# Kernel tuning notes

Hardware: AMD Instinct MI355X
Metric: run time of the kernel (lower is better)

The kernel has to match this reference:

```python
import jax, jax.numpy as jnp
import numpy as np
from jax import lax

B, T, I, H = 262144, 10, 1, 32


def setup_inputs() -> dict:
    key = jax.random.key(0)
    ks = jax.random.split(key, 7)
    s_ih = 1.0 / np.sqrt(H)
    return {
        "x": jax.random.normal(ks[0], (B, T, I), dtype=jnp.float32),
        "h0": jnp.zeros((1, B, H), dtype=jnp.float32),
        "Wih": jax.random.uniform(ks[1], (H, I), minval=-s_ih, maxval=s_ih, dtype=jnp.float32),
        "Whh": jax.random.uniform(ks[2], (H, H), minval=-s_ih, maxval=s_ih, dtype=jnp.float32),
        "bih": jax.random.uniform(ks[3], (H,), minval=-s_ih, maxval=s_ih, dtype=jnp.float32),
        "bhh": jax.random.uniform(ks[4], (H,), minval=-s_ih, maxval=s_ih, dtype=jnp.float32),
        "Wout": jax.random.uniform(ks[5], (1, H), minval=-s_ih, maxval=s_ih, dtype=jnp.float32),
        "bout": jax.random.uniform(ks[6], (1,), minval=-s_ih, maxval=s_ih, dtype=jnp.float32),
    }


def reference(x, h0, Wih, Whh, bih, bhh, Wout, bout):
    # Elman RNN: h_t = tanh(x_t Wih^T + bih + h_{t-1} Whh^T + bhh)
    # Precompute the input projection for all timesteps (batched GEMM),
    # then scan the sequential recurrence over T.
    xW = jnp.einsum("bti,hi->tbh", x, Wih) + (bih + bhh)  # [T,B,H]

    def step(h, xw_t):
        h_new = jnp.tanh(xw_t + h @ Whh.T)
        return h_new, h_new

    h_last, hs = lax.scan(step, h0[0], xW)  # hs: [T,B,H]
    r_out = jnp.swapaxes(hs, 0, 1)  # [B,T,H]
    outs = r_out @ Wout.T + bout    # fused linear head, [B,T,1]
    return outs, h_last[None]       # match (outs.view(-1,T,1), h_state[1,B,H])
```

## Files before the change

### kernel.cpp

```cpp
#include <hip/hip_runtime.h>


#define RNN_T 10
#define RNN_H 32

typedef __attribute__((ext_vector_type(4))) unsigned int u32x4;
typedef __attribute__((ext_vector_type(8))) short s16x8;
typedef __attribute__((ext_vector_type(16))) float f32x16;

static __device__ __forceinline__ float fast_tanh(float a) {
    float ez = __builtin_amdgcn_exp2f(a * 2.885390081777927f);
    float r  = __builtin_amdgcn_rcpf(ez + 1.0f);
    return fmaf(-2.0f, r, 1.0f);
}

static __device__ __forceinline__ unsigned pack_hi_pair(float f0, float f1) {
    return (__float_as_uint(f1) & 0xffff0000u) | (__float_as_uint(f0) >> 16);
}
static __device__ __forceinline__ float trunc_bf16_f32(float f) {
    return __uint_as_float(__float_as_uint(f) & 0xffff0000u);
}

static __device__ __forceinline__ f32x16 mfma_bf16(u32x4 a, u32x4 b, f32x16 c) {
    return __builtin_amdgcn_mfma_f32_32x32x16_bf16(
        __builtin_bit_cast(s16x8, a), __builtin_bit_cast(s16x8, b), c, 0, 0, 0);
}

static __device__ __forceinline__ void load_split8(const float* __restrict__ p,
                                                   u32x4& hi4, u32x4& lo4) {
    float4 w0 = *reinterpret_cast<const float4*>(p);
    float4 w1 = *reinterpret_cast<const float4*>(p + 4);
    float w[8] = {w0.x, w0.y, w0.z, w0.w, w1.x, w1.y, w1.z, w1.w};
    #pragma unroll
    for (int i = 0; i < 4; ++i) {
        float f0 = w[2 * i], f1 = w[2 * i + 1];
        hi4[i] = pack_hi_pair(f0, f1);
        lo4[i] = pack_hi_pair(f0 - trunc_bf16_f32(f0), f1 - trunc_bf16_f32(f1));
    }
}

__global__ __launch_bounds__(256) void rnn_mfma(
    const float* __restrict__ x,
    const float* __restrict__ h0,
    const float* __restrict__ Wih,
    const float* __restrict__ Whh,
    const float* __restrict__ bih,
    const float* __restrict__ bhh,
    const float* __restrict__ Wout,
    const float* __restrict__ bout,
    float* __restrict__ out,
    int B)
{
    const int tid  = threadIdx.x;
    const int lane = tid & 63;
    const int l31  = lane & 31;
    const int hi   = lane >> 5;
    const bool lo_lane = (hi == 0);
    const int wave = tid >> 6;
    const int tile = blockIdx.x * 4 + wave;
    const int b    = tile * 32 + l31;
    const int kb   = hi * 8;

    u32x4 A1h, A1l, A2h, A2l;
    load_split8(Whh + l31 * RNN_H + 0  + kb, A1h, A1l);
    load_split8(Whh + l31 * RNN_H + 16 + kb, A2h, A2l);

    u32x4 B1h, B1l, B2h, B2l;
    load_split8(h0 + (size_t)b * RNN_H + 0  + kb, B1h, B1l);
    load_split8(h0 + (size_t)b * RNN_H + 16 + kb, B2h, B2l);

    float wih_r[16], bias_r[16], wout_r[16];
    #pragma unroll
    for (int r = 0; r < 16; ++r) {
        int row = (r & 3) + 8 * (r >> 2) + 4 * hi;
        wih_r[r]  = Wih[row];
        bias_r[r] = bih[row] + bhh[row];
        wout_r[r] = Wout[row];
    }

    float xw[RNN_T];
    #pragma unroll
    for (int t = 0; t < RNN_T; ++t) xw[t] = x[(size_t)b * RNN_T + t];

    const float bo = bout[0];
    float h[16];

    #pragma unroll
    for (int t = 0; t < RNN_T; ++t) {
        f32x16 acc;
        #pragma unroll
        for (int r = 0; r < 16; ++r) acc[r] = fmaf(xw[t], wih_r[r], bias_r[r]);

        acc = mfma_bf16(A1h, B1h, acc);
        acc = mfma_bf16(A2h, B2h, acc);
        acc = mfma_bf16(A1h, B1l, acc);
        acc = mfma_bf16(A2h, B2l, acc);
        acc = mfma_bf16(A1l, B1h, acc);
        acc = mfma_bf16(A2l, B2h, acc);
        acc = mfma_bf16(A1l, B1l, acc);
        acc = mfma_bf16(A2l, B2l, acc);

        #pragma unroll
        for (int r = 0; r < 16; ++r) h[r] = fast_tanh(acc[r]);

        float o = 0.f;
        #pragma unroll
        for (int r = 0; r < 16; ++r) o = fmaf(h[r], wout_r[r], o);
        o += __shfl_xor(o, 32);
        if (lane < 32) out[(size_t)b * RNN_T + t] = o + bo;

        if (t < RNN_T - 1) {
            unsigned Sh[8], Sl[8];
            #pragma unroll
            for (int p = 0; p < 8; ++p) {
                float f0 = h[2 * p], f1 = h[2 * p + 1];
                Sh[p] = pack_hi_pair(f0, f1);
                Sl[p] = pack_hi_pair(f0 - trunc_bf16_f32(f0),
                                     f1 - trunc_bf16_f32(f1));
            }
            unsigned r0h = __shfl_xor(lo_lane ? Sh[2] : Sh[0], 32);
            unsigned r1h = __shfl_xor(lo_lane ? Sh[3] : Sh[1], 32);
            unsigned r2h = __shfl_xor(lo_lane ? Sh[6] : Sh[4], 32);
            unsigned r3h = __shfl_xor(lo_lane ? Sh[7] : Sh[5], 32);
            unsigned r0l = __shfl_xor(lo_lane ? Sl[2] : Sl[0], 32);
            unsigned r1l = __shfl_xor(lo_lane ? Sl[3] : Sl[1], 32);
            unsigned r2l = __shfl_xor(lo_lane ? Sl[6] : Sl[4], 32);
            unsigned r3l = __shfl_xor(lo_lane ? Sl[7] : Sl[5], 32);
            B1h[0] = lo_lane ? Sh[0] : r0h;  B1h[1] = lo_lane ? Sh[1] : r1h;
            B1h[2] = lo_lane ? r0h : Sh[2];  B1h[3] = lo_lane ? r1h : Sh[3];
            B2h[0] = lo_lane ? Sh[4] : r2h;  B2h[1] = lo_lane ? Sh[5] : r3h;
            B2h[2] = lo_lane ? r2h : Sh[6];  B2h[3] = lo_lane ? r3h : Sh[7];
            B1l[0] = lo_lane ? Sl[0] : r0l;  B1l[1] = lo_lane ? Sl[1] : r1l;
            B1l[2] = lo_lane ? r0l : Sl[2];  B1l[3] = lo_lane ? r1l : Sl[3];
            B2l[0] = lo_lane ? Sl[4] : r2l;  B2l[1] = lo_lane ? Sl[5] : r3l;
            B2l[2] = lo_lane ? r2l : Sl[6];  B2l[3] = lo_lane ? r3l : Sl[7];
        }
    }

    float* hl = out + (size_t)B * RNN_T + (size_t)b * RNN_H;
    #pragma unroll
    for (int q = 0; q < 4; ++q) {
        float4 v;
        v.x = h[4 * q + 0]; v.y = h[4 * q + 1];
        v.z = h[4 * q + 2]; v.w = h[4 * q + 3];
        *reinterpret_cast<float4*>(hl + 8 * q + 4 * hi) = v;
    }
}

extern "C" void kernel_launch(void* const* d_in, const int* in_sizes, int n_in,
                              void* d_out, int out_size, void* d_ws, size_t ws_size,
                              hipStream_t stream) {
    const float* x    = (const float*)d_in[0];
    const float* h0   = (const float*)d_in[1];
    const float* Wih  = (const float*)d_in[2];
    const float* Whh  = (const float*)d_in[3];
    const float* bih  = (const float*)d_in[4];
    const float* bhh  = (const float*)d_in[5];
    const float* Wout = (const float*)d_in[6];
    const float* bout = (const float*)d_in[7];
    float* out = (float*)d_out;

    const int B = in_sizes[1] / RNN_H;
    dim3 grid(B / 128);
    dim3 block(256);
    hipLaunchKernelGGL(rnn_mfma, grid, block, 0, stream,
                       x, h0, Wih, Whh, bih, bhh, Wout, bout, out, B);
}
```

Baseline: 134.4 us.

## Interleave two batch tiles per wave, use permlane32 swaps, drop lo*lo MFMA terms

Each wave now processes two 32-row batch tiles with interleaved MFMA chains, so the two independent dependency chains can hide MFMA and tanh latency. Cross-half exchanges move from shfl_xor with selects to v_permlane32_swap, and the two lowest-order bf16 split products (A_lo*B_lo) are dropped, leaving six MFMAs per tile instead of eight. The time loop is no longer unrolled, and x is prefetched one step ahead instead of loaded up front. The grid is halved. Dropping the lo*lo terms slightly reduces precision, and there are fewer waves to hide latency.

```diff
diff --git a/kernel.cpp b/kernel.cpp
--- a/kernel.cpp
+++ b/kernel.cpp
@@ -39,9 +39,22 @@
     }
 }
 
-__global__ __launch_bounds__(256) void rnn_mfma(
+static __device__ __forceinline__ void swap32(unsigned& xv, unsigned& yv) {
+    asm volatile("v_permlane32_swap_b32 %0, %1" : "+v"(xv), "+v"(yv));
+}
+
+static __device__ __forceinline__ void rebuild(const unsigned S[8],
+                                               u32x4& Bk1, u32x4& Bk2) {
+    unsigned a, b;
+    a = S[0]; b = S[2]; swap32(a, b); Bk1[0] = a; Bk1[2] = b;
+    a = S[1]; b = S[3]; swap32(a, b); Bk1[1] = a; Bk1[3] = b;
+    a = S[4]; b = S[6]; swap32(a, b); Bk2[0] = a; Bk2[2] = b;
+    a = S[5]; b = S[7]; swap32(a, b); Bk2[1] = a; Bk2[3] = b;
+}
+
+__global__ __launch_bounds__(256) void rnn_mfma2(
     const float* __restrict__ x,
-    const float* __restrict__ h0,
+    const float* __restrict__ hin,
     const float* __restrict__ Wih,
     const float* __restrict__ Whh,
     const float* __restrict__ bih,
@@ -55,19 +68,20 @@
     const int lane = tid & 63;
     const int l31  = lane & 31;
     const int hi   = lane >> 5;
-    const bool lo_lane = (hi == 0);
     const int wave = tid >> 6;
-    const int tile = blockIdx.x * 4 + wave;
-    const int b    = tile * 32 + l31;
+    const int b0   = (blockIdx.x * 8 + wave * 2) * 32 + l31;
+    const int b1   = b0 + 32;
     const int kb   = hi * 8;
 
     u32x4 A1h, A1l, A2h, A2l;
-    load_split8(Whh + l31 * RNN_H + 0  + kb, A1h, A1l);
+    load_split8(Whh + l31 * RNN_H + kb,      A1h, A1l);
     load_split8(Whh + l31 * RNN_H + 16 + kb, A2h, A2l);
 
-    u32x4 B1h, B1l, B2h, B2l;
-    load_split8(h0 + (size_t)b * RNN_H + 0  + kb, B1h, B1l);
-    load_split8(h0 + (size_t)b * RNN_H + 16 + kb, B2h, B2l);
+    u32x4 B1h0, B1l0, B2h0, B2l0, B1h1, B1l1, B2h1, B2l1;
+    load_split8(hin + (size_t)b0 * RNN_H + kb,      B1h0, B1l0);
+    load_split8(hin + (size_t)b0 * RNN_H + 16 + kb, B2h0, B2l0);
+    load_split8(hin + (size_t)b1 * RNN_H + kb,      B1h1, B1l1);
+    load_split8(hin + (size_t)b1 * RNN_H + 16 + kb, B2h1, B2l1);
 
     float wih_r[16], bias_r[16], wout_r[16];
     #pragma unroll
@@ -78,72 +92,83 @@
         wout_r[r] = Wout[row];
     }
 
-    float xw[RNN_T];
-    #pragma unroll
-    for (int t = 0; t < RNN_T; ++t) xw[t] = x[(size_t)b * RNN_T + t];
+    const float bo = bout[0];
+    const float* xp0 = x + (size_t)b0 * RNN_T;
+    const float* xp1 = x + (size_t)b1 * RNN_T;
+    float* op0 = out + (size_t)b0 * RNN_T;
+    float* op1 = out + (size_t)b1 * RNN_T;
 
-    const float bo = bout[0];
-    float h[16];
+    float h0r[16], h1r[16];
+    float xc0 = xp0[0], xc1 = xp1[0];
 
-    #pragma unroll
+    #pragma unroll 1
     for (int t = 0; t < RNN_T; ++t) {
-        f32x16 acc;
+        const int tn = (t < RNN_T - 1) ? t + 1 : t;
+        const float xn0 = xp0[tn], xn1 = xp1[tn];
+
+        f32x16 acc0, acc1;
         #pragma unroll
-        for (int r = 0; r < 16; ++r) acc[r] = fmaf(xw[t], wih_r[r], bias_r[r]);
-
-        acc = mfma_bf16(A1h, B1h, acc);
-        acc = mfma_bf16(A2h, B2h, acc);
-        acc = mfma_bf16(A1h, B1l, acc);
-        acc = mfma_bf16(A2h, B2l, acc);
-        acc = mfma_bf16(A1l, B1h, acc);
-        acc = mfma_bf16(A2l, B2h, acc);
-        acc = mfma_bf16(A1l, B1l, acc);
-        acc = mfma_bf16(A2l, B2l, acc);
+        for (int r = 0; r < 16; ++r) {
+            acc0[r] = fmaf(xc0, wih_r[r], bias_r[r]);
+            acc1[r] = fmaf(xc1, wih_r[r], bias_r[r]);
+        }
+        acc0 = mfma_bf16(A1h, B1h0, acc0);  acc1 = mfma_bf16(A1h, B1h1, acc1);
+        acc0 = mfma_bf16(A2h, B2h0, acc0);  acc1 = mfma_bf16(A2h, B2h1, acc1);
+        acc0 = mfma_bf16(A1h, B1l0, acc0);  acc1 = mfma_bf16(A1h, B1l1, acc1);
+        acc0 = mfma_bf16(A2h, B2l0, acc0);  acc1 = mfma_bf16(A2h, B2l1, acc1);
+        acc0 = mfma_bf16(A1l, B1h0, acc0);  acc1 = mfma_bf16(A1l, B1h1, acc1);
+        acc0 = mfma_bf16(A2l, B2h0, acc0);  acc1 = mfma_bf16(A2l, B2h1, acc1);
 
         #pragma unroll
-        for (int r = 0; r < 16; ++r) h[r] = fast_tanh(acc[r]);
+        for (int r = 0; r < 16; ++r) {
+            h0r[r] = fast_tanh(acc0[r]);
+            h1r[r] = fast_tanh(acc1[r]);
+        }
 
-        float o = 0.f;
+        float o0 = 0.f, o1 = 0.f;
         #pragma unroll
-        for (int r = 0; r < 16; ++r) o = fmaf(h[r], wout_r[r], o);
-        o += __shfl_xor(o, 32);
-        if (lane < 32) out[(size_t)b * RNN_T + t] = o + bo;
+        for (int r = 0; r < 16; ++r) {
+            o0 = fmaf(h0r[r], wout_r[r], o0);
+            o1 = fmaf(h1r[r], wout_r[r], o1);
+        }
+        unsigned oa0 = __float_as_uint(o0), ob0 = oa0;
+        unsigned oa1 = __float_as_uint(o1), ob1 = oa1;
+        swap32(oa0, ob0);
+        swap32(oa1, ob1);
+        if (lane < 32) {
+            op0[t] = __uint_as_float(oa0) + __uint_as_float(ob0) + bo;
+            op1[t] = __uint_as_float(oa1) + __uint_as_float(ob1) + bo;
+        }
 
-        if (t < RNN_T - 1) {
-            unsigned Sh[8], Sl[8];
-            #pragma unroll
-            for (int p = 0; p < 8; ++p) {
-                float f0 = h[2 * p], f1 = h[2 * p + 1];
-                Sh[p] = pack_hi_pair(f0, f1);
-                Sl[p] = pack_hi_pair(f0 - trunc_bf16_f32(f0),
-                                     f1 - trunc_bf16_f32(f1));
-            }
-            unsigned r0h = __shfl_xor(lo_lane ? Sh[2] : Sh[0], 32);
-            unsigned r1h = __shfl_xor(lo_lane ? Sh[3] : Sh[1], 32);
-            unsigned r2h = __shfl_xor(lo_lane ? Sh[6] : Sh[4], 32);
-            unsigned r3h = __shfl_xor(lo_lane ? Sh[7] : Sh[5], 32);
-            unsigned r0l = __shfl_xor(lo_lane ? Sl[2] : Sl[0], 32);
-            unsigned r1l = __shfl_xor(lo_lane ? Sl[3] : Sl[1], 32);
-            unsigned r2l = __shfl_xor(lo_lane ? Sl[6] : Sl[4], 32);
-            unsigned r3l = __shfl_xor(lo_lane ? Sl[7] : Sl[5], 32);
-            B1h[0] = lo_lane ? Sh[0] : r0h;  B1h[1] = lo_lane ? Sh[1] : r1h;
-            B1h[2] = lo_lane ? r0h : Sh[2];  B1h[3] = lo_lane ? r1h : Sh[3];
-            B2h[0] = lo_lane ? Sh[4] : r2h;  B2h[1] = lo_lane ? Sh[5] : r3h;
-            B2h[2] = lo_lane ? r2h : Sh[6];  B2h[3] = lo_lane ? r3h : Sh[7];
-            B1l[0] = lo_lane ? Sl[0] : r0l;  B1l[1] = lo_lane ? Sl[1] : r1l;
-            B1l[2] = lo_lane ? r0l : Sl[2];  B1l[3] = lo_lane ? r1l : Sl[3];
-            B2l[0] = lo_lane ? Sl[4] : r2l;  B2l[1] = lo_lane ? Sl[5] : r3l;
-            B2l[2] = lo_lane ? r2l : Sl[6];  B2l[3] = lo_lane ? r3l : Sl[7];
+        unsigned Sh[8], Sl[8];
+        #pragma unroll
+        for (int p = 0; p < 8; ++p) {
+            float f0 = h0r[2 * p], f1 = h0r[2 * p + 1];
+            Sh[p] = pack_hi_pair(f0, f1);
+            Sl[p] = pack_hi_pair(f0 - trunc_bf16_f32(f0), f1 - trunc_bf16_f32(f1));
         }
+        rebuild(Sh, B1h0, B2h0);
+        rebuild(Sl, B1l0, B2l0);
+        #pragma unroll
+        for (int p = 0; p < 8; ++p) {
+            float f0 = h1r[2 * p], f1 = h1r[2 * p + 1];
+            Sh[p] = pack_hi_pair(f0, f1);
+            Sl[p] = pack_hi_pair(f0 - trunc_bf16_f32(f0), f1 - trunc_bf16_f32(f1));
+        }
+        rebuild(Sh, B1h1, B2h1);
+        rebuild(Sl, B1l1, B2l1);
+
+        xc0 = xn0; xc1 = xn1;
     }
 
-    float* hl = out + (size_t)B * RNN_T + (size_t)b * RNN_H;
+    float* hl0 = out + (size_t)B * RNN_T + (size_t)b0 * RNN_H;
+    float* hl1 = out + (size_t)B * RNN_T + (size_t)b1 * RNN_H;
     #pragma unroll
     for (int q = 0; q < 4; ++q) {
-        float4 v;
-        v.x = h[4 * q + 0]; v.y = h[4 * q + 1];
-        v.z = h[4 * q + 2]; v.w = h[4 * q + 3];
-        *reinterpret_cast<float4*>(hl + 8 * q + 4 * hi) = v;
+        float4 v0 = make_float4(h0r[4*q], h0r[4*q+1], h0r[4*q+2], h0r[4*q+3]);
+        float4 v1 = make_float4(h1r[4*q], h1r[4*q+1], h1r[4*q+2], h1r[4*q+3]);
+        *reinterpret_cast<float4*>(hl0 + 8 * q + 4 * hi) = v0;
+        *reinterpret_cast<float4*>(hl1 + 8 * q + 4 * hi) = v1;
     }
 }
 
@@ -161,8 +186,8 @@
     float* out = (float*)d_out;
 
     const int B = in_sizes[1] / RNN_H;
-    dim3 grid(B / 128);
+    dim3 grid(B / 256);
     dim3 block(256);
-    hipLaunchKernelGGL(rnn_mfma, grid, block, 0, stream,
+    hipLaunchKernelGGL(rnn_mfma2, grid, block, 0, stream,
                        x, h0, Wih, Whh, bih, bhh, Wout, bout, out, B);
 }
```

Result: slower. 140.6 us (+4.6%).
